# Kernel optimization log

Measured on AMD Instinct MI355X. Metric: run time of the kernel, lower is better.

Reference implementation:

```python
import jax, jax.numpy as jnp
import numpy as np

T, N, F = 96, 1140, 64   # timesteps, nodes per graph, node feature dim
H = 32                    # GAT hidden channels
LH = 250                  # LSTM hidden
OUT = 2280                # per-head output
E = 22800                 # edges per graph


def setup_inputs() -> dict:
    key = jax.random.key(0)
    ks = jax.random.split(key, 32)
    s = lambda k, shape, fan: jax.random.normal(k, shape, jnp.float32) / np.sqrt(fan)
    inp = {}
    inp["nodes"] = jax.random.normal(ks[0], (T, N, F), jnp.float32)
    inp["edges_index"] = jax.random.randint(ks[1], (T, 2, E), 0, N)
    inp["edges_attr"] = jax.random.normal(ks[2], (T, E), jnp.float32)  # unused by forward (faithful)
    # GAT layer 1 (F -> H) and layer 2 (H -> H), heads=1
    inp["gat_W1"] = s(ks[3], (F, H), F)
    inp["gat_as1"] = s(ks[4], (H,), H)
    inp["gat_ad1"] = s(ks[5], (H,), H)
    inp["gat_b1"] = jnp.zeros((H,), jnp.float32)
    inp["gat_W2"] = s(ks[6], (H, H), H)
    inp["gat_as2"] = s(ks[7], (H,), H)
    inp["gat_ad2"] = s(ks[8], (H,), H)
    inp["gat_b2"] = jnp.zeros((H,), jnp.float32)
    # 2-layer LSTM, batch_first, batch=1, input = N*H
    IN0 = N * H
    inp["Wih0"] = s(ks[9], (4 * LH, IN0), IN0)
    inp["Whh0"] = s(ks[10], (4 * LH, LH), LH)
    inp["bih0"] = jnp.zeros((4 * LH,), jnp.float32)
    inp["bhh0"] = jnp.zeros((4 * LH,), jnp.float32)
    inp["Wih1"] = s(ks[11], (4 * LH, LH), LH)
    inp["Whh1"] = s(ks[12], (4 * LH, LH), LH)
    inp["bih1"] = jnp.zeros((4 * LH,), jnp.float32)
    inp["bhh1"] = jnp.zeros((4 * LH,), jnp.float32)
    # random initial states (original uses torch.randn in forward)
    inp["h0"] = jax.random.normal(ks[13], (2, 1, LH), jnp.float32)
    inp["c0"] = jax.random.normal(ks[14], (2, 1, LH), jnp.float32)
    for i in range(4):
        inp[f"fc{i+1}_W"] = s(ks[15 + 2 * i], (OUT, LH), LH)
        inp[f"fc{i+1}_b"] = jnp.zeros((OUT,), jnp.float32)
    return inp


def _gat_conv(x, src, dst, W, a_s, a_d, b, n):
    # GATConv, heads=1: h = xW; e_ij = LeakyReLU(a_s.h_src + a_d.h_dst);
    # softmax over edges sharing a destination; scatter-add aggregation.
    h = x @ W                                                   # [N, H]
    e = jax.nn.leaky_relu((h @ a_s)[src] + (h @ a_d)[dst], negative_slope=0.2)
    m = jax.ops.segment_max(e, dst, num_segments=n)
    ex = jnp.exp(e - m[dst])
    denom = jax.ops.segment_sum(ex, dst, num_segments=n)
    alpha = ex / denom[dst]
    return jax.ops.segment_sum(alpha[:, None] * h[src], dst, num_segments=n) + b


def _lstm_layer(xs, Wih, Whh, bih, bhh, h0, c0):
    # xs: [T, B, in]; torch gate order i, f, g, o
    def step(carry, x):
        h, c = carry
        g = x @ Wih.T + h @ Whh.T + bih + bhh
        i, f, gg, o = jnp.split(g, 4, axis=-1)
        c = jax.nn.sigmoid(f) * c + jax.nn.sigmoid(i) * jnp.tanh(gg)
        h = jax.nn.sigmoid(o) * jnp.tanh(c)
        return (h, c), h
    (_, _), ys = jax.lax.scan(step, (h0, c0), xs)
    return ys


def reference(nodes, edges_index, edges_attr, gat_W1, gat_as1, gat_ad1, gat_b1,
              gat_W2, gat_as2, gat_ad2, gat_b2,
              Wih0, Whh0, bih0, bhh0, Wih1, Whh1, bih1, bhh1, h0, c0,
              fc1_W, fc1_b, fc2_W, fc2_b, fc3_W, fc3_b, fc4_W, fc4_b):
    n = nodes.shape[1]
    loop = jnp.arange(n)  # self-loops (GATConv default add_self_loops=True)

    def per_graph(x, ei):
        src = jnp.concatenate([ei[0], loop])
        dst = jnp.concatenate([ei[1], loop])
        h = jax.nn.relu(_gat_conv(x, src, dst, gat_W1, gat_as1, gat_ad1, gat_b1, n))
        h = _gat_conv(h, src, dst, gat_W2, gat_as2, gat_ad2, gat_b2, n)
        return h.reshape(-1)

    seq = jax.vmap(per_graph)(nodes, edges_index)   # [T, N*H]
    xs = seq[:, None, :]                            # [T, 1, N*H] (batch=1)
    ys = _lstm_layer(xs, Wih0, Whh0, bih0, bhh0, h0[0], c0[0])
    ys = _lstm_layer(ys, Wih1, Whh1, bih1, bhh1, h0[1], c0[1])
    last = ys[-1]                                   # [1, LH]
    preds = [last @ fc1_W.T + fc1_b, last @ fc2_W.T + fc2_b,
             last @ fc3_W.T + fc3_b, last @ fc4_W.T + fc4_b]
    return jnp.stack(preds, axis=0).reshape(last.shape[0], 4, -1)  # [1, 4, 2280]
```

## Files before the change

### kernel.cpp

```cpp
#include <hip/hip_runtime.h>

#define T_ 96
#define N_ 1140
#define F_ 64
#define H_ 32
#define E_ 22800
#define LH_ 250
#define G4_ 1000
#define OUT_ 2280
#define KIN_ 36480
#define SPLITK 60
#define KC 32
#define BN 32

typedef _Float16 h2_t __attribute__((ext_vector_type(2)));

__device__ __forceinline__ float leaky02(float x){ return x > 0.f ? x : 0.2f*x; }
__device__ __forceinline__ float fsigm(float x){ return 1.f/(1.f + __expf(-x)); }
__device__ __forceinline__ float ftanh(float x){
  x = fminf(fmaxf(x, -15.f), 15.f);
  float t = __expf(2.f * x);
  return (t - 1.f) / (t + 1.f);
}
__device__ __forceinline__ unsigned packh2(float a, float b) {
  auto p = __builtin_amdgcn_cvt_pkrtz(a, b);
  return __builtin_bit_cast(unsigned, p);
}
__device__ __forceinline__ float fdot2u(unsigned w, unsigned h, float acc) {
  return __builtin_amdgcn_fdot2(__builtin_bit_cast(h2_t, w),
                                __builtin_bit_cast(h2_t, h), acc, false);
}

__device__ __forceinline__ void st_agent_u(unsigned* p, unsigned v) {
  __hip_atomic_store(p, v, __ATOMIC_RELAXED, __HIP_MEMORY_SCOPE_AGENT);
}
__device__ __forceinline__ unsigned ld_agent_u(const unsigned* p) {
  return __hip_atomic_load((unsigned*)p, __ATOMIC_RELAXED, __HIP_MEMORY_SCOPE_AGENT);
}
__device__ __forceinline__ void st_agent_i(int* p, int v) {
  __hip_atomic_store(p, v, __ATOMIC_RELAXED, __HIP_MEMORY_SCOPE_AGENT);
}
__device__ __forceinline__ int ld_agent_i(const int* p) {
  return __hip_atomic_load((int*)p, __ATOMIC_RELAXED, __HIP_MEMORY_SCOPE_AGENT);
}

__global__ void k_feat(const float* __restrict__ x, const float* __restrict__ W,
                       const float* __restrict__ as_, const float* __restrict__ ad_,
                       float* __restrict__ Hout, float* __restrict__ HS,
                       float* __restrict__ HD, int K) {
  int gid = blockIdx.x * blockDim.x + threadIdx.x;
  int row = gid >> 5; int c = gid & 31;
  if (row >= T_ * N_) return;
  const float* xr = x + (size_t)row * K;
  float acc = 0.f;
  for (int k = 0; k < K; ++k) acc += xr[k] * W[k * H_ + c];
  Hout[(size_t)row * H_ + c] = acc;
  float ps = acc * as_[c], pd = acc * ad_[c];
  #pragma unroll
  for (int off = 16; off > 0; off >>= 1) {
    ps += __shfl_xor(ps, off, 32);
    pd += __shfl_xor(pd, off, 32);
  }
  if (c == 0) { HS[row] = ps; HD[row] = pd; }
}

__global__ void k_count(const int* __restrict__ ei, int* __restrict__ counts) {
  int gid = blockIdx.x * blockDim.x + threadIdx.x;
  if (gid >= T_ * E_) return;
  int t = gid / E_; int k = gid - t * E_;
  int dst = ei[(size_t)t * 2 * E_ + E_ + k];
  atomicAdd(&counts[t * N_ + dst], 1);
}

__global__ void k_scan(const int* __restrict__ counts, int* __restrict__ offs,
                       int* __restrict__ cursor) {
  int t = blockIdx.x; int tid = threadIdx.x;
  int base = tid * 5;
  int v[5]; int s = 0;
  #pragma unroll
  for (int r = 0; r < 5; ++r) {
    int i = base + r;
    int c = (i < N_) ? counts[t * N_ + i] : 0;
    v[r] = c; s += c;
  }
  __shared__ int sh[256];
  sh[tid] = s; __syncthreads();
  for (int off = 1; off < 256; off <<= 1) {
    int add = (tid >= off) ? sh[tid - off] : 0;
    __syncthreads();
    sh[tid] += add;
    __syncthreads();
  }
  int run = sh[tid] - s;
  #pragma unroll
  for (int r = 0; r < 5; ++r) {
    int i = base + r;
    if (i < N_) { offs[t * (N_ + 1) + i] = run; cursor[t * N_ + i] = run; }
    run += v[r];
  }
  if (tid == 255) offs[t * (N_ + 1) + N_] = sh[255];
}

__global__ void k_fill(const int* __restrict__ ei, int* __restrict__ cursor,
                       int* __restrict__ elist) {
  int gid = blockIdx.x * blockDim.x + threadIdx.x;
  if (gid >= T_ * E_) return;
  int t = gid / E_; int k = gid - t * E_;
  int src = ei[(size_t)t * 2 * E_ + k];
  int dst = ei[(size_t)t * 2 * E_ + E_ + k];
  int pos = atomicAdd(&cursor[t * N_ + dst], 1);
  elist[(size_t)t * E_ + pos] = src;
}

__global__ void k_aggr(const float* __restrict__ Hf, const float* __restrict__ HS,
                       const float* __restrict__ HD, const int* __restrict__ offs,
                       const int* __restrict__ elist, const float* __restrict__ b,
                       float* __restrict__ Xout, int relu) {
  int gid = blockIdx.x * blockDim.x + threadIdx.x;
  int row = gid >> 5; int c = gid & 31;
  if (row >= T_ * N_) return;
  int t = row / N_; int i = row - t * N_;
  float hd_i = HD[row];
  float m = leaky02(HS[row] + hd_i);
  float s = 1.f;
  float acc = Hf[(size_t)row * H_ + c];
  int e0 = offs[t * (N_ + 1) + i], e1 = offs[t * (N_ + 1) + i + 1];
  const int* el = elist + (size_t)t * E_;
  const float* Ht = Hf + (size_t)t * N_ * H_;
  const float* HSt = HS + t * N_;
  float hsA = 0.f, hvA = 0.f;
  if (e0 < e1) {
    int srcA = el[e0];
    hsA = HSt[srcA];
    hvA = Ht[(size_t)srcA * H_ + c];
  }
  for (int e = e0; e < e1; ++e) {
    float hs = hsA, hv = hvA;
    if (e + 1 < e1) {
      int srcA = el[e + 1];
      hsA = HSt[srcA];
      hvA = Ht[(size_t)srcA * H_ + c];
    }
    float eg = leaky02(hs + hd_i);
    float mn = fmaxf(m, eg);
    float scl = __expf(m - mn);
    float p = __expf(eg - mn);
    s = s * scl + p;
    acc = acc * scl + p * hv;
    m = mn;
  }
  float val = acc / s + b[c];
  if (relu) val = fmaxf(val, 0.f);
  Xout[(size_t)row * H_ + c] = val;
}

__global__ void k_gemm(const float* __restrict__ X, const float* __restrict__ Wih,
                       float* __restrict__ Gpart) {
  __shared__ unsigned Xs[T_][KC / 2 + 1];
  __shared__ unsigned Ws[BN][KC / 2 + 1];
  int j0 = blockIdx.x * BN;
  int sp = blockIdx.y;
  int tid = threadIdx.x;
  int jj = tid & 7;
  int tt = tid >> 3;
  float acc[6][4] = {};
  int kbeg = sp * (KIN_ / SPLITK);
  int kend = kbeg + (KIN_ / SPLITK);
  for (int k0 = kbeg; k0 < kend; k0 += KC) {
    for (int idx = tid; idx < T_ * (KC / 2); idx += 128) {
      int tr = idx >> 4; int kk = idx & 15;
      const float2 v = *(const float2*)(X + (size_t)tr * KIN_ + k0 + 2 * kk);
      Xs[tr][kk] = packh2(v.x, v.y);
    }
    for (int idx = tid; idx < BN * (KC / 2); idx += 128) {
      int jr = idx >> 4; int kk = idx & 15;
      int j = j0 + jr;
      unsigned v = 0;
      if (j < G4_) {
        const float2 w = *(const float2*)(Wih + (size_t)j * KIN_ + k0 + 2 * kk);
        v = packh2(w.x, w.y);
      }
      Ws[jr][kk] = v;
    }
    __syncthreads();
    for (int kk = 0; kk < KC / 2; ++kk) {
      unsigned xv[6], wv[4];
      #pragma unroll
      for (int r = 0; r < 6; ++r) xv[r] = Xs[tt * 6 + r][kk];
      #pragma unroll
      for (int q = 0; q < 4; ++q) wv[q] = Ws[jj * 4 + q][kk];
      #pragma unroll
      for (int r = 0; r < 6; ++r)
        #pragma unroll
        for (int q = 0; q < 4; ++q)
          acc[r][q] = fdot2u(wv[q], xv[r], acc[r][q]);
    }
    __syncthreads();
  }
  #pragma unroll
  for (int r = 0; r < 6; ++r) {
    int t = tt * 6 + r;
    #pragma unroll
    for (int q = 0; q < 4; ++q) {
      int j = j0 + jj * 4 + q;
      if (j < G4_) Gpart[((size_t)sp * T_ + t) * 1024 + j] = acc[r][q];
    }
  }
}

__global__ void k_gred(const float* __restrict__ Gpart, const float* __restrict__ bih,
                       const float* __restrict__ bhh, float* __restrict__ G0) {
  int idx = blockIdx.x * blockDim.x + threadIdx.x;
  if (idx >= T_ * G4_) return;
  int t = idx / G4_; int jg = idx - t * G4_;
  int j = jg >> 2, g = jg & 3;
  int c = g * LH_ + j;
  float s = bih[c] + bhh[c];
  for (int sp = 0; sp < SPLITK; ++sp) s += Gpart[((size_t)sp * T_ + t) * 1024 + c];
  G0[idx] = s;
}

__global__ void __launch_bounds__(512, 2) k_lstm(
    const float* __restrict__ G0, const float* __restrict__ Whh0,
    const float* __restrict__ Wih1, const float* __restrict__ Whh1,
    const float* __restrict__ bih1, const float* __restrict__ bhh1,
    const float* __restrict__ h0in, const float* __restrict__ c0in,
    unsigned* __restrict__ hp,
    int* __restrict__ flags,
    float* __restrict__ ylast) {
  int tid = threadIdx.x;
  int bid = blockIdx.x;
  int wv = bid * 8 + (tid >> 6);
  int lane = tid & 63;
  int qg = lane >> 4;
  int ql = lane & 15;

  unsigned w0[4][8], wx1[4][8], wh1[4][8];
  float bs1[4], c0l[4], c1l[4];
  bool act[4];
  #pragma unroll
  for (int u = 0; u < 4; ++u) {
    int U = wv * 4 + u;
    act[u] = (U < LH_);
    int Uc = act[u] ? U : 0;
    size_t rb = (size_t)(qg * LH_ + Uc) * LH_;
    #pragma unroll
    for (int m = 0; m < 8; ++m) {
      int pi = m * 16 + ql;
      if (act[u] && pi < 125) {
        w0[u][m]  = packh2(Whh0[rb + 2 * pi], Whh0[rb + 2 * pi + 1]);
        wx1[u][m] = packh2(Wih1[rb + 2 * pi], Wih1[rb + 2 * pi + 1]);
        wh1[u][m] = packh2(Whh1[rb + 2 * pi], Whh1[rb + 2 * pi + 1]);
      } else { w0[u][m] = 0; wx1[u][m] = 0; wh1[u][m] = 0; }
    }
    bs1[u] = act[u] ? (bih1[qg * LH_ + Uc] + bhh1[qg * LH_ + Uc]) : 0.f;
    c0l[u] = act[u] ? c0in[Uc] : 0.f;
    c1l[u] = act[u] ? c0in[LH_ + Uc] : 0.f;
  }

  float gpre[4];
  #pragma unroll
  for (int u = 0; u < 4; ++u)
    gpre[u] = act[u] ? G0[0 * G4_ + (wv * 4 + u) * 4 + qg] : 0.f;

  for (int p = 0; p <= T_; ++p) {
    int rs = (p - 1) & 1, wslot = p & 1;
    unsigned x0p[8], h1p[8];
    if (p == 0) {
      #pragma unroll
      for (int m = 0; m < 8; ++m) {
        int pi = m * 16 + ql;
        x0p[m] = (pi < 125) ? packh2(h0in[2 * pi], h0in[2 * pi + 1]) : 0u;
      }
    } else {
      #pragma unroll
      for (int m = 0; m < 8; ++m)
        x0p[m] = ld_agent_u(&hp[rs * 256 + m * 16 + ql]);
      if (p == 1) {
        #pragma unroll
        for (int m = 0; m < 8; ++m) {
          int pi = m * 16 + ql;
          h1p[m] = (pi < 125) ? packh2(h0in[LH_ + 2 * pi], h0in[LH_ + 2 * pi + 1]) : 0u;
        }
      } else {
        #pragma unroll
        for (int m = 0; m < 8; ++m)
          h1p[m] = ld_agent_u(&hp[rs * 256 + 128 + m * 16 + ql]);
      }
    }

    if (p < T_) {
      float h0new[4];
      #pragma unroll
      for (int u = 0; u < 4; ++u) {
        float s = 0.f;
        #pragma unroll
        for (int m = 0; m < 8; ++m) s = fdot2u(w0[u][m], x0p[m], s);
        s += __shfl_xor(s, 1); s += __shfl_xor(s, 2);
        s += __shfl_xor(s, 4); s += __shfl_xor(s, 8);
        float pre = s + gpre[u];
        float a = (qg == 2) ? ftanh(pre) : fsigm(pre);
        float ai = __shfl(a, ql);
        float af = __shfl(a, 16 + ql);
        float ag = __shfl(a, 32 + ql);
        float ao = __shfl(a, 48 + ql);
        c0l[u] = af * c0l[u] + ai * ag;
        h0new[u] = act[u] ? (ao * ftanh(c0l[u])) : 0.f;
      }
      if (lane == 0) {
        st_agent_u(&hp[wslot * 256 + 2 * wv],     packh2(h0new[0], h0new[1]));
        st_agent_u(&hp[wslot * 256 + 2 * wv + 1], packh2(h0new[2], h0new[3]));
      }
    }
    if (p >= 1) {
      float h1new[4];
      #pragma unroll
      for (int u = 0; u < 4; ++u) {
        float s = 0.f;
        #pragma unroll
        for (int m = 0; m < 8; ++m) s = fdot2u(wx1[u][m], x0p[m], s);
        #pragma unroll
        for (int m = 0; m < 8; ++m) s = fdot2u(wh1[u][m], h1p[m], s);
        s += __shfl_xor(s, 1); s += __shfl_xor(s, 2);
        s += __shfl_xor(s, 4); s += __shfl_xor(s, 8);
        float pre = s + bs1[u];
        float a = (qg == 2) ? ftanh(pre) : fsigm(pre);
        float bi = __shfl(a, ql);
        float bf = __shfl(a, 16 + ql);
        float bg = __shfl(a, 32 + ql);
        float bo = __shfl(a, 48 + ql);
        c1l[u] = bf * c1l[u] + bi * bg;
        h1new[u] = act[u] ? (bo * ftanh(c1l[u])) : 0.f;
      }
      if (p - 1 == T_ - 1 && lane == 0) {
        #pragma unroll
        for (int u = 0; u < 4; ++u)
          if (act[u]) ylast[wv * 4 + u] = h1new[u];
      }
      if (lane == 0) {
        st_agent_u(&hp[wslot * 256 + 128 + 2 * wv],     packh2(h1new[0], h1new[1]));
        st_agent_u(&hp[wslot * 256 + 128 + 2 * wv + 1], packh2(h1new[2], h1new[3]));
      }
    }
    float gnext[4];
    #pragma unroll
    for (int u = 0; u < 4; ++u)
      gnext[u] = (p + 1 < T_ && act[u]) ? G0[(p + 1) * G4_ + (wv * 4 + u) * 4 + qg] : 0.f;
    if (p < T_) {
      __syncthreads();
      if (tid == 0) {
        asm volatile("s_waitcnt vmcnt(0)" ::: "memory");
        st_agent_i(&flags[bid], p + 1);
      }
      if (tid < 64) {
        int guard = 0;
        for (;;) {
          int f = ld_agent_i(&flags[lane & 7]);
          if (__ballot(f >= p + 1) == ~0ULL) break;
          if (++guard > (1 << 22)) break;
          __builtin_amdgcn_s_sleep(1);
        }
      }
      __syncthreads();
    }
    #pragma unroll
    for (int u = 0; u < 4; ++u) gpre[u] = gnext[u];
  }
}

__global__ void k_fc(const float* __restrict__ ylast,
                     const float* __restrict__ Wa, const float* __restrict__ ba,
                     const float* __restrict__ Wb, const float* __restrict__ bb,
                     const float* __restrict__ Wc, const float* __restrict__ bc,
                     const float* __restrict__ Wd, const float* __restrict__ bd,
                     float* __restrict__ out) {
  int wg = blockIdx.x * 4 + (threadIdx.x >> 6);
  int lane = threadIdx.x & 63;
  if (wg >= 4 * OUT_) return;
  int head = wg / OUT_, o = wg - head * OUT_;
  const float* W = head == 0 ? Wa : head == 1 ? Wb : head == 2 ? Wc : Wd;
  const float* b = head == 0 ? ba : head == 1 ? bb : head == 2 ? bc : bd;
  float s = 0.f;
  #pragma unroll
  for (int r = 0; r < 4; ++r) {
    int idx = r * 64 + lane;
    if (idx < LH_) s += ylast[idx] * W[(size_t)o * LH_ + idx];
  }
  #pragma unroll
  for (int off = 32; off > 0; off >>= 1) s += __shfl_xor(s, off, 64);
  if (lane == 0) out[wg] = s + b[o];
}

extern "C" void kernel_launch(void* const* d_in, const int* in_sizes, int n_in,
                              void* d_out, int out_size, void* d_ws, size_t ws_size,
                              hipStream_t stream) {
  const float* nodes = (const float*)d_in[0];
  const int*   ei    = (const int*)d_in[1];
  const float* W1    = (const float*)d_in[3];
  const float* as1   = (const float*)d_in[4];
  const float* ad1   = (const float*)d_in[5];
  const float* b1    = (const float*)d_in[6];
  const float* W2    = (const float*)d_in[7];
  const float* as2   = (const float*)d_in[8];
  const float* ad2   = (const float*)d_in[9];
  const float* b2    = (const float*)d_in[10];
  const float* Wih0  = (const float*)d_in[11];
  const float* Whh0  = (const float*)d_in[12];
  const float* bih0  = (const float*)d_in[13];
  const float* bhh0  = (const float*)d_in[14];
  const float* Wih1  = (const float*)d_in[15];
  const float* Whh1  = (const float*)d_in[16];
  const float* bih1  = (const float*)d_in[17];
  const float* bhh1  = (const float*)d_in[18];
  const float* h0    = (const float*)d_in[19];
  const float* c0    = (const float*)d_in[20];
  const float* fW1   = (const float*)d_in[21];
  const float* fb1   = (const float*)d_in[22];
  const float* fW2   = (const float*)d_in[23];
  const float* fb2   = (const float*)d_in[24];
  const float* fW3   = (const float*)d_in[25];
  const float* fb3   = (const float*)d_in[26];
  const float* fW4   = (const float*)d_in[27];
  const float* fb4   = (const float*)d_in[28];
  float* out = (float*)d_out;

  const size_t o_Gpart  = 0;
  const size_t o_H      = 0;
  const size_t o_HS     = 14008320;
  const size_t o_HD     = 14446080;
  const size_t o_X1     = 14883840;
  const size_t o_X2     = 28892160;
  const size_t o_counts = 42900480;
  const size_t o_offs   = 43338240;
  const size_t o_cursor = 43776512;
  const size_t o_elist  = 44214272;
  const size_t o_G0     = 52969472;
  const size_t o_hp     = 53353472;
  const size_t o_flags  = 53355520;
  const size_t o_ylast  = 53355776;
  const size_t total    = 53356800;
  if (ws_size < total) return;

  char* ws = (char*)d_ws;
  float*    Gpart  = (float*)(ws + o_Gpart);
  float*    Hbuf   = (float*)(ws + o_H);
  float*    HS     = (float*)(ws + o_HS);
  float*    HD     = (float*)(ws + o_HD);
  float*    X1     = (float*)(ws + o_X1);
  float*    X2     = (float*)(ws + o_X2);
  int*      counts = (int*)(ws + o_counts);
  int*      offs   = (int*)(ws + o_offs);
  int*      cursor = (int*)(ws + o_cursor);
  int*      elist  = (int*)(ws + o_elist);
  float*    G0     = (float*)(ws + o_G0);
  unsigned* hp     = (unsigned*)(ws + o_hp);
  int*      flags  = (int*)(ws + o_flags);
  float*    ylast  = (float*)(ws + o_ylast);

  (void)hipMemsetAsync(counts, 0, (size_t)T_ * N_ * 4, stream);
  (void)hipMemsetAsync(hp, 0, 2048, stream);
  (void)hipMemsetAsync(flags, 0, 256, stream);

  const int rows_grid = (T_ * N_ * H_) / 256;
  const int eg = (T_ * E_ + 255) / 256;

  k_feat<<<rows_grid, 256, 0, stream>>>(nodes, W1, as1, ad1, Hbuf, HS, HD, F_);
  k_count<<<eg, 256, 0, stream>>>(ei, counts);
  k_scan<<<T_, 256, 0, stream>>>(counts, offs, cursor);
  k_fill<<<eg, 256, 0, stream>>>(ei, cursor, elist);
  k_aggr<<<rows_grid, 256, 0, stream>>>(Hbuf, HS, HD, offs, elist, b1, X1, 1);
  k_feat<<<rows_grid, 256, 0, stream>>>(X1, W2, as2, ad2, Hbuf, HS, HD, H_);
  k_aggr<<<rows_grid, 256, 0, stream>>>(Hbuf, HS, HD, offs, elist, b2, X2, 0);
  k_gemm<<<dim3(32, SPLITK), 128, 0, stream>>>(X2, Wih0, Gpart);
  k_gred<<<(T_ * G4_ + 255) / 256, 256, 0, stream>>>(Gpart, bih0, bhh0, G0);
  k_lstm<<<8, 512, 0, stream>>>(G0, Whh0, Wih1, Whh1, bih1, bhh1, h0, c0,
                                hp, flags, ylast);
  k_fc<<<OUT_, 256, 0, stream>>>(ylast, fW1, fb1, fW2, fb2, fW3, fb3, fW4, fb4, out);
}
```

Measured before the change: 1.196 ms.

## Co-locate LSTM workgroups on one XCD and use workgroup-scope atomics for step sync

The LSTM kernel now launches 256 workgroups. Each reads its XCC_ID, and the eight that land on XCD 0 become the active workers if enough are present; otherwise it falls back to the first eight arrivals using agent-scope operations. When co-located, cross-workgroup hidden-state exchange and step flags go through workgroup-scope atomic RMW ops, which avoids agent-level coherence round trips. The per-step barrier is replaced by a single-wave poll on split layer-0 and layer-1 flags, with the data staged through LDS, so producers no longer wait for consumers. The scheme relies on hardware placement behaviour, and the extra workgroups cost some launch overhead.

```diff
diff --git a/kernel.cpp b/kernel.cpp
--- a/kernel.cpp
+++ b/kernel.cpp
@@ -12,8 +12,10 @@
 #define SPLITK 60
 #define KC 32
 #define BN 32
+#define NWG_LSTM 256
 
 typedef _Float16 h2_t __attribute__((ext_vector_type(2)));
+typedef unsigned long long u64;
 
 __device__ __forceinline__ float leaky02(float x){ return x > 0.f ? x : 0.2f*x; }
 __device__ __forceinline__ float fsigm(float x){ return 1.f/(1.f + __expf(-x)); }
@@ -31,17 +33,21 @@
                                 __builtin_bit_cast(h2_t, h), acc, false);
 }
 
-__device__ __forceinline__ void st_agent_u(unsigned* p, unsigned v) {
-  __hip_atomic_store(p, v, __ATOMIC_RELAXED, __HIP_MEMORY_SCOPE_AGENT);
-}
-__device__ __forceinline__ unsigned ld_agent_u(const unsigned* p) {
-  return __hip_atomic_load((unsigned*)p, __ATOMIC_RELAXED, __HIP_MEMORY_SCOPE_AGENT);
-}
-__device__ __forceinline__ void st_agent_i(int* p, int v) {
-  __hip_atomic_store(p, v, __ATOMIC_RELAXED, __HIP_MEMORY_SCOPE_AGENT);
-}
-__device__ __forceinline__ int ld_agent_i(const int* p) {
-  return __hip_atomic_load((int*)p, __ATOMIC_RELAXED, __HIP_MEMORY_SCOPE_AGENT);
+__device__ __forceinline__ int poll_i(int* p, int mode, int z) {
+  if (mode == 1) return __hip_atomic_fetch_add(p, z, __ATOMIC_RELAXED, __HIP_MEMORY_SCOPE_WORKGROUP);
+  return __hip_atomic_load(p, __ATOMIC_RELAXED, __HIP_MEMORY_SCOPE_AGENT);
+}
+__device__ __forceinline__ u64 poll_u64(u64* p, int mode, u64 z) {
+  if (mode == 1) return __hip_atomic_fetch_add(p, z, __ATOMIC_RELAXED, __HIP_MEMORY_SCOPE_WORKGROUP);
+  return __hip_atomic_load(p, __ATOMIC_RELAXED, __HIP_MEMORY_SCOPE_AGENT);
+}
+__device__ __forceinline__ void post_u32(unsigned* p, unsigned v, int mode) {
+  if (mode == 1) (void)__hip_atomic_exchange(p, v, __ATOMIC_RELAXED, __HIP_MEMORY_SCOPE_WORKGROUP);
+  else __hip_atomic_store(p, v, __ATOMIC_RELAXED, __HIP_MEMORY_SCOPE_AGENT);
+}
+__device__ __forceinline__ void post_i(int* p, int v, int mode) {
+  if (mode == 1) (void)__hip_atomic_exchange(p, v, __ATOMIC_RELAXED, __HIP_MEMORY_SCOPE_WORKGROUP);
+  else __hip_atomic_store(p, v, __ATOMIC_RELAXED, __HIP_MEMORY_SCOPE_AGENT);
 }
 
 __global__ void k_feat(const float* __restrict__ x, const float* __restrict__ W,
@@ -226,12 +232,55 @@
     const float* __restrict__ bih1, const float* __restrict__ bhh1,
     const float* __restrict__ h0in, const float* __restrict__ c0in,
     unsigned* __restrict__ hp,
-    int* __restrict__ flags,
+    int* __restrict__ sync,
     float* __restrict__ ylast) {
+  __shared__ __align__(8) unsigned ldsX[128];
+  __shared__ __align__(8) unsigned ldsH1[128];
+  __shared__ int sh_role, sh_mode;
+
   int tid = threadIdx.x;
-  int bid = blockIdx.x;
-  int wv = bid * 8 + (tid >> 6);
+  if (tid == 0) {
+    int xcd;
+    asm volatile("s_getreg_b32 %0, hwreg(HW_REG_XCC_ID)" : "=s"(xcd));
+    xcd &= 7;
+    int r = -1;
+    if (xcd == 0)
+      r = __hip_atomic_fetch_add(&sync[0], 1, __ATOMIC_RELAXED, __HIP_MEMORY_SCOPE_AGENT);
+    int g = __hip_atomic_fetch_add(&sync[8], 1, __ATOMIC_RELAXED, __HIP_MEMORY_SCOPE_AGENT);
+    if (g == 0) {
+      int guard = 0;
+      while (__hip_atomic_load(&sync[8], __ATOMIC_RELAXED, __HIP_MEMORY_SCOPE_AGENT) < NWG_LSTM
+             && ++guard < (1 << 22)) __builtin_amdgcn_s_sleep(2);
+      int c0 = __hip_atomic_load(&sync[0], __ATOMIC_RELAXED, __HIP_MEMORY_SCOPE_AGENT);
+      int md = (c0 >= 8) ? 1 : 2;
+      __hip_atomic_store(&sync[9], 4 | md, __ATOMIC_RELAXED, __HIP_MEMORY_SCOPE_AGENT);
+    }
+    int mv, guard = 0;
+    for (;;) {
+      mv = __hip_atomic_load(&sync[9], __ATOMIC_RELAXED, __HIP_MEMORY_SCOPE_AGENT);
+      if (mv & 4) break;
+      if (++guard > (1 << 22)) { mv = 4 | 2; break; }
+      __builtin_amdgcn_s_sleep(2);
+    }
+    int mode = mv & 3;
+    int role;
+    if (mode == 1) role = (xcd == 0 && r >= 0 && r < 8) ? r : -1;
+    else           role = (g < 8) ? g : -1;
+    sh_role = role; sh_mode = mode;
+  }
+  __syncthreads();
+  int role = sh_role, mode = sh_mode;
+  if (role < 0) return;
+
+  int* flags0 = sync + 16;
+  int* flags1 = sync + 24;
+  u64* hp64 = (u64*)hp;
+  int z = sync[15];
+  u64 zu = (u64)(unsigned)z;
+
+  int wave = tid >> 6;
   int lane = tid & 63;
+  int wv = role * 8 + wave;
   int qg = lane >> 4;
   int ql = lane & 15;
 
@@ -264,18 +313,36 @@
     gpre[u] = act[u] ? G0[0 * G4_ + (wv * 4 + u) * 4 + qg] : 0.f;
 
   for (int p = 0; p <= T_; ++p) {
-    int rs = (p - 1) & 1, wslot = p & 1;
     unsigned x0p[8], h1p[8];
     if (p == 0) {
       #pragma unroll
       for (int m = 0; m < 8; ++m) {
         int pi = m * 16 + ql;
         x0p[m] = (pi < 125) ? packh2(h0in[2 * pi], h0in[2 * pi + 1]) : 0u;
+        h1p[m] = 0u;
       }
     } else {
-      #pragma unroll
-      for (int m = 0; m < 8; ++m)
-        x0p[m] = ld_agent_u(&hp[rs * 256 + m * 16 + ql]);
+      if (wave == 0) {
+        int i8 = lane & 7;
+        int need1 = (p >= 2) ? (p - 1) : 0;
+        int guard = 0;
+        for (;;) {
+          int f0 = poll_i(&flags0[i8], mode, z);
+          int f1 = (p >= 2) ? poll_i(&flags1[i8], mode, z) : need1;
+          if (__all(f0 >= p && f1 >= need1)) break;
+          if (++guard > (1 << 22)) break;
+          __builtin_amdgcn_s_sleep(1);
+        }
+        u64 xv = poll_u64(&hp64[(size_t)((p - 1) & 1) * 128 + lane], mode, zu);
+        ((u64*)ldsX)[lane] = xv;
+        if (p >= 2) {
+          u64 hv = poll_u64(&hp64[(size_t)(p & 1) * 128 + 64 + lane], mode, zu);
+          ((u64*)ldsH1)[lane] = hv;
+        }
+      }
+      __syncthreads();
+      #pragma unroll
+      for (int m = 0; m < 8; ++m) x0p[m] = ldsX[m * 16 + ql];
       if (p == 1) {
         #pragma unroll
         for (int m = 0; m < 8; ++m) {
@@ -284,8 +351,7 @@
         }
       } else {
         #pragma unroll
-        for (int m = 0; m < 8; ++m)
-          h1p[m] = ld_agent_u(&hp[rs * 256 + 128 + m * 16 + ql]);
+        for (int m = 0; m < 8; ++m) h1p[m] = ldsH1[m * 16 + ql];
       }
     }
 
@@ -307,9 +373,11 @@
         c0l[u] = af * c0l[u] + ai * ag;
         h0new[u] = act[u] ? (ao * ftanh(c0l[u])) : 0.f;
       }
-      if (lane == 0) {
-        st_agent_u(&hp[wslot * 256 + 2 * wv],     packh2(h0new[0], h0new[1]));
-        st_agent_u(&hp[wslot * 256 + 2 * wv + 1], packh2(h0new[2], h0new[3]));
+      int w = 2 * wv + lane;
+      if (lane < 2 && w < 125) {
+        unsigned pair = (lane == 0) ? packh2(h0new[0], h0new[1])
+                                    : packh2(h0new[2], h0new[3]);
+        post_u32(&hp[(size_t)(p & 1) * 256 + w], pair, mode);
       }
     }
     if (p >= 1) {
@@ -332,14 +400,19 @@
         c1l[u] = bf * c1l[u] + bi * bg;
         h1new[u] = act[u] ? (bo * ftanh(c1l[u])) : 0.f;
       }
-      if (p - 1 == T_ - 1 && lane == 0) {
-        #pragma unroll
-        for (int u = 0; u < 4; ++u)
-          if (act[u]) ylast[wv * 4 + u] = h1new[u];
-      }
-      if (lane == 0) {
-        st_agent_u(&hp[wslot * 256 + 128 + 2 * wv],     packh2(h1new[0], h1new[1]));
-        st_agent_u(&hp[wslot * 256 + 128 + 2 * wv + 1], packh2(h1new[2], h1new[3]));
+      if (p - 1 == T_ - 1) {
+        if (lane == 0) {
+          #pragma unroll
+          for (int u = 0; u < 4; ++u)
+            if (act[u]) ylast[wv * 4 + u] = h1new[u];
+        }
+      } else {
+        int w = 2 * wv + lane;
+        if (lane < 2 && w < 125) {
+          unsigned pair = (lane == 0) ? packh2(h1new[0], h1new[1])
+                                      : packh2(h1new[2], h1new[3]);
+          post_u32(&hp[(size_t)((p - 1) & 1) * 256 + 128 + w], pair, mode);
+        }
       }
     }
     float gnext[4];
@@ -350,18 +423,9 @@
       __syncthreads();
       if (tid == 0) {
         asm volatile("s_waitcnt vmcnt(0)" ::: "memory");
-        st_agent_i(&flags[bid], p + 1);
-      }
-      if (tid < 64) {
-        int guard = 0;
-        for (;;) {
-          int f = ld_agent_i(&flags[lane & 7]);
-          if (__ballot(f >= p + 1) == ~0ULL) break;
-          if (++guard > (1 << 22)) break;
-          __builtin_amdgcn_s_sleep(1);
-        }
-      }
-      __syncthreads();
+        post_i(&flags0[role], p + 1, mode);
+        if (p >= 1) post_i(&flags1[role], p, mode);
+      }
     }
     #pragma unroll
     for (int u = 0; u < 4; ++u) gpre[u] = gnext[u];
@@ -436,7 +500,7 @@
   const size_t o_elist  = 44214272;
   const size_t o_G0     = 52969472;
   const size_t o_hp     = 53353472;
-  const size_t o_flags  = 53355520;
+  const size_t o_sync   = 53355520;
   const size_t o_ylast  = 53355776;
   const size_t total    = 53356800;
   if (ws_size < total) return;
@@ -454,12 +518,12 @@
   int*      elist  = (int*)(ws + o_elist);
   float*    G0     = (float*)(ws + o_G0);
   unsigned* hp     = (unsigned*)(ws + o_hp);
-  int*      flags  = (int*)(ws + o_flags);
+  int*      syncA  = (int*)(ws + o_sync);
   float*    ylast  = (float*)(ws + o_ylast);
 
   (void)hipMemsetAsync(counts, 0, (size_t)T_ * N_ * 4, stream);
   (void)hipMemsetAsync(hp, 0, 2048, stream);
-  (void)hipMemsetAsync(flags, 0, 256, stream);
+  (void)hipMemsetAsync(syncA, 0, 256, stream);
 
   const int rows_grid = (T_ * N_ * H_) / 256;
   const int eg = (T_ * E_ + 255) / 256;
@@ -473,7 +537,7 @@
   k_aggr<<<rows_grid, 256, 0, stream>>>(Hbuf, HS, HD, offs, elist, b2, X2, 0);
   k_gemm<<<dim3(32, SPLITK), 128, 0, stream>>>(X2, Wih0, Gpart);
   k_gred<<<(T_ * G4_ + 255) / 256, 256, 0, stream>>>(Gpart, bih0, bhh0, G0);
-  k_lstm<<<8, 512, 0, stream>>>(G0, Whh0, Wih1, Whh1, bih1, bhh1, h0, c0,
-                                hp, flags, ylast);
+  k_lstm<<<NWG_LSTM, 512, 0, stream>>>(G0, Whh0, Wih1, Whh1, bih1, bhh1, h0, c0,
+                                       hp, syncA, ylast);
   k_fc<<<OUT_, 256, 0, stream>>>(ylast, fW1, fb1, fW2, fb2, fW3, fb3, fW4, fb4, out);
 }
```

Measured after the change: 1.445 ms. 1.21x slower.
